# Kernel tuning notes

Hardware: AMD Instinct MI355X
Metric: run time of the kernel (lower is better)

Reference implementation:

```python
import jax, jax.numpy as jnp
import numpy as np

EMBED = 768
HEADS = 8
HEAD_DIM = EMBED // HEADS  # 96


def setup_inputs() -> dict:
    key = jax.random.key(0)
    k1, k2, k3, k4, k5 = jax.random.split(key, 5)
    b, n = 4, 2048
    x = jax.random.normal(k1, (b, n, EMBED), dtype=jnp.float32)
    s = 1.0 / np.sqrt(EMBED)
    W_qkv = jax.random.normal(k2, (EMBED, 3 * EMBED), dtype=jnp.float32) * s
    b_qkv = jax.random.normal(k3, (3 * EMBED,), dtype=jnp.float32) * 0.02
    W_proj = jax.random.normal(k4, (EMBED, EMBED), dtype=jnp.float32) * s
    b_proj = jax.random.normal(k5, (EMBED,), dtype=jnp.float32) * 0.02
    return {"x": x, "W_qkv": W_qkv, "b_qkv": b_qkv, "W_proj": W_proj, "b_proj": b_proj}


def reference(x, W_qkv, b_qkv, W_proj, b_proj):
    b, n, _ = x.shape
    qkv = x @ W_qkv + b_qkv  # [b, n, 3*EMBED]
    # rearrange 'b n (h d qkv) -> qkv b h n d': qkv is fastest-varying axis
    qkv = qkv.reshape(b, n, HEADS, HEAD_DIM, 3)
    q = jnp.transpose(qkv[..., 0], (0, 2, 1, 3))  # [b, h, n, d]
    k = jnp.transpose(qkv[..., 1], (0, 2, 1, 3))
    v = jnp.transpose(qkv[..., 2], (0, 2, 1, 3))
    scale = 1.0 / np.sqrt(HEAD_DIM)
    energy = jnp.einsum('bhqd,bhkd->bhqk', q, k) * scale
    attn = jax.nn.softmax(energy, axis=-1)  # dropout p=0 -> identity
    out = jnp.einsum('bhqk,bhkd->bhqd', attn, v)
    out = jnp.transpose(out, (0, 2, 1, 3)).reshape(b, n, EMBED)
    out = out @ W_proj + b_proj
    return out
```

## Files before the change

kernel.cpp:

```cpp
#include <hip/hip_runtime.h>
#include <hip/hip_bf16.h>

#define EMBED 768
#define NHEADS 8
#define HDIM 96
#define SEQ 2048
#define BATCH 4
#define NTOK (BATCH*SEQ)
#define QKVN (3*EMBED)

#define QSCALE 0.14724444f

typedef __attribute__((ext_vector_type(4))) float f32x4;
typedef __attribute__((ext_vector_type(8))) __bf16 bf16x8;

__device__ __forceinline__ unsigned short f2bf(float f) {
  union { float f; unsigned int u; } c; c.f = f;
  unsigned int u = c.u;
  return (unsigned short)((u + 0x7FFFu + ((u >> 16) & 1u)) >> 16);
}

__device__ __forceinline__ void gload_lds16(const void* g, void* l) {
  __builtin_amdgcn_global_load_lds(
      (const __attribute__((address_space(1))) unsigned int*)g,
      (__attribute__((address_space(3))) unsigned int*)l, 16, 0, 0);
}

__global__ __launch_bounds__(256) void cast_x_kernel(const float4* __restrict__ in,
                                                     ushort4* __restrict__ out, int n4) {
  int i = blockIdx.x * 256 + threadIdx.x;
  if (i >= n4) return;
  float4 v = in[i];
  out[i] = make_ushort4(f2bf(v.x), f2bf(v.y), f2bf(v.z), f2bf(v.w));
}

__global__ __launch_bounds__(256) void transpose_cast_kernel(const float* __restrict__ in,
                                                             unsigned short* __restrict__ out,
                                                             int R, int C) {
  __shared__ float t[32][33];
  int c0 = blockIdx.x * 32, r0 = blockIdx.y * 32;
  int tx = threadIdx.x & 31, ty = threadIdx.x >> 5;
  #pragma unroll
  for (int i = 0; i < 32; i += 8)
    t[ty + i][tx] = in[(size_t)(r0 + ty + i) * C + c0 + tx];
  __syncthreads();
  #pragma unroll
  for (int i = 0; i < 32; i += 8)
    out[(size_t)(c0 + ty + i) * R + r0 + tx] = f2bf(t[tx][ty + i]);
}

template <int MODE>
__global__ __launch_bounds__(256) void gemm_kernel(
    const unsigned short* __restrict__ A, const unsigned short* __restrict__ B,
    const float* __restrict__ bias, int K,
    unsigned short* __restrict__ Qo, unsigned short* __restrict__ Ko,
    unsigned short* __restrict__ Vt, float* __restrict__ out) {
  __shared__ unsigned short As[2][128][32];
  __shared__ unsigned short Bs[2][128][32];
  const int tid = threadIdx.x;
  const int lane = tid & 63, wid = tid >> 6;
  const int wr = wid >> 1, wc = wid & 1;
  const int l15 = lane & 15, l16 = lane >> 4;
  const int m0 = blockIdx.y * 128, n0 = blockIdx.x * 128;

  auto stage = [&](int buf, int k0) {
    #pragma unroll
    for (int i = 0; i < 2; i++) {
      int chunk = i * 256 + tid;
      gload_lds16(A + (size_t)(m0 + (chunk >> 2)) * K + k0 + (chunk & 3) * 8,
                  (char*)&As[buf][0][0] + (i * 256 + wid * 64) * 16);
      gload_lds16(B + (size_t)(n0 + (chunk >> 2)) * K + k0 + (chunk & 3) * 8,
                  (char*)&Bs[buf][0][0] + (i * 256 + wid * 64) * 16);
    }
  };

  f32x4 acc[4][4] = {};

  stage(0, 0);
  __syncthreads();
  int cur = 0;
  for (int k0 = 0; k0 < K; k0 += 32, cur ^= 1) {
    if (k0 + 32 < K) stage(cur ^ 1, k0 + 32);

    bf16x8 af[4], bfr[4];
    #pragma unroll
    for (int mi = 0; mi < 4; mi++)
      af[mi] = *(const bf16x8*)&As[cur][wr * 64 + mi * 16 + l15][l16 * 8];
    #pragma unroll
    for (int ni = 0; ni < 4; ni++)
      bfr[ni] = *(const bf16x8*)&Bs[cur][wc * 64 + ni * 16 + l15][l16 * 8];
    #pragma unroll
    for (int mi = 0; mi < 4; mi++)
      #pragma unroll
      for (int ni = 0; ni < 4; ni++)
        acc[mi][ni] = __builtin_amdgcn_mfma_f32_16x16x32_bf16(af[mi], bfr[ni], acc[mi][ni], 0, 0, 0);

    __syncthreads();
  }

  if (MODE == 0) {
    #pragma unroll
    for (int mi = 0; mi < 4; mi++) {
      #pragma unroll
      for (int ni = 0; ni < 4; ni++) {
        int col = n0 + wc * 64 + ni * 16 + l15;
        int h = col / 288;
        int rem = col - h * 288;
        int d = rem / 3;
        int which = rem - d * 3;
        float bb = bias[col];
        #pragma unroll
        for (int j = 0; j < 4; j++) {
          int row = m0 + wr * 64 + mi * 16 + l16 * 4 + j;
          int bi = row >> 11, nn = row & 2047;
          float v = acc[mi][ni][j] + bb;
          size_t bh = (size_t)(bi * NHEADS + h);
          if (which == 0)      Qo[(bh * SEQ + nn) * HDIM + d] = f2bf(v * QSCALE);
          else if (which == 1) Ko[(bh * SEQ + nn) * HDIM + d] = f2bf(v);
          else                 Vt[(bh * HDIM + d) * SEQ + nn] = f2bf(v);
        }
      }
    }
  } else {
    #pragma unroll
    for (int mi = 0; mi < 4; mi++) {
      #pragma unroll
      for (int ni = 0; ni < 4; ni++) {
        int col = n0 + wc * 64 + ni * 16 + l15;
        float bb = bias[col];
        #pragma unroll
        for (int j = 0; j < 4; j++) {
          int row = m0 + wr * 64 + mi * 16 + l16 * 4 + j;
          out[(size_t)row * EMBED + col] = acc[mi][ni][j] + bb;
        }
      }
    }
  }
}

__global__ __launch_bounds__(256) void attn_kernel(
    const unsigned short* __restrict__ Q, const unsigned short* __restrict__ Kd,
    const unsigned short* __restrict__ Vt, unsigned short* __restrict__ Oa) {
  __shared__ unsigned short Ks[64 * 96];
  __shared__ unsigned short Vs[96 * 64];
  __shared__ unsigned short Ps[4][32 * 64];

  const int tid = threadIdx.x, lane = tid & 63, wid = tid >> 6;
  const int l15 = lane & 15, l16 = lane >> 4;
  const int bid = blockIdx.x;
  const int swz = (bid & 7) * 64 + (bid >> 3);
  const int qb_ = swz & 15, bh = swz >> 4;
  const int bi = bh >> 3, h = bh & 7;
  const int q0 = qb_ * 128;

  const unsigned short* Qg = Q + ((size_t)bh * SEQ + q0) * HDIM;
  const unsigned short* Kg = Kd + (size_t)bh * SEQ * HDIM;
  const unsigned short* Vg = Vt + (size_t)bh * HDIM * SEQ;

  bf16x8 qf[2][3];
  #pragma unroll
  for (int qb = 0; qb < 2; qb++)
    #pragma unroll
    for (int ks = 0; ks < 3; ks++)
      qf[qb][ks] = *(const bf16x8*)(Qg + (size_t)(wid * 32 + qb * 16 + l15) * HDIM + ks * 32 + l16 * 8);

  auto stageKV = [&](int k0) {
    #pragma unroll
    for (int i = 0; i < 3; i++) {
      int idx = i * 256 + tid;
      gload_lds16(Kg + (size_t)k0 * HDIM + idx * 8,
                  (char*)Ks + (i * 256 + wid * 64) * 16);
    }
    #pragma unroll
    for (int i = 0; i < 3; i++) {
      int idx = i * 256 + tid;
      int d = idx >> 3, slot = idx & 7;
      gload_lds16(Vg + (size_t)d * SEQ + k0 + ((slot ^ (d & 7)) << 3),
                  (char*)Vs + (i * 256 + wid * 64) * 16);
    }
  };

  f32x4 oacc[2][6] = {};
  float mrow[2], lrow[2];
  mrow[0] = mrow[1] = -__builtin_inff();
  lrow[0] = lrow[1] = 0.f;

  char* pw = (char*)&Ps[wid][0];
  const int swzP = ((l15 & 7) << 4) ^ ((l15 & 8) << 2);

  for (int kb = 0; kb < SEQ / 64; kb++) {
    __syncthreads();
    stageKV(kb * 64);
    __syncthreads();

    f32x4 sacc[2][4] = {};
    #pragma unroll
    for (int ks = 0; ks < 3; ks++) {
      bf16x8 ak[4];
      #pragma unroll
      for (int ni = 0; ni < 4; ni++)
        ak[ni] = *(const bf16x8*)((const char*)Ks + (ni * 16 + l15) * 192 + ks * 64 + l16 * 16);
      #pragma unroll
      for (int qb = 0; qb < 2; qb++)
        #pragma unroll
        for (int ni = 0; ni < 4; ni++)
          sacc[qb][ni] = __builtin_amdgcn_mfma_f32_16x16x32_bf16(ak[ni], qf[qb][ks], sacc[qb][ni], 0, 0, 0);
    }

    float tmax[2];
    float g = -3.4e38f;
    #pragma unroll
    for (int qb = 0; qb < 2; qb++) {
      float v = fmaxf(
          fmaxf(fmaxf(fmaxf(sacc[qb][0][0], sacc[qb][0][1]), fmaxf(sacc[qb][0][2], sacc[qb][0][3])),
                fmaxf(fmaxf(sacc[qb][1][0], sacc[qb][1][1]), fmaxf(sacc[qb][1][2], sacc[qb][1][3]))),
          fmaxf(fmaxf(fmaxf(sacc[qb][2][0], sacc[qb][2][1]), fmaxf(sacc[qb][2][2], sacc[qb][2][3])),
                fmaxf(fmaxf(sacc[qb][3][0], sacc[qb][3][1]), fmaxf(sacc[qb][3][2], sacc[qb][3][3]))));
      v = fmaxf(v, __shfl_xor(v, 16));
      v = fmaxf(v, __shfl_xor(v, 32));
      tmax[qb] = v;
      g = fmaxf(g, v - mrow[qb]);
    }
    if (!__all(g <= 11.54f)) {
      #pragma unroll
      for (int qb = 0; qb < 2; qb++) {
        float mnew = fmaxf(mrow[qb], tmax[qb]);
        float alpha = __builtin_amdgcn_exp2f(mrow[qb] - mnew);
        mrow[qb] = mnew;
        lrow[qb] *= alpha;
        #pragma unroll
        for (int d6 = 0; d6 < 6; d6++) {
          oacc[qb][d6][0] *= alpha; oacc[qb][d6][1] *= alpha;
          oacc[qb][d6][2] *= alpha; oacc[qb][d6][3] *= alpha;
        }
      }
    }

    #pragma unroll
    for (int qb = 0; qb < 2; qb++) {
      const float m = mrow[qb];
      char* rowp = pw + (qb * 16 + l15) * 128;
      float psum = 0.f;
      #pragma unroll
      for (int ni = 0; ni < 4; ni++) {
        float p0 = __builtin_amdgcn_exp2f(sacc[qb][ni][0] - m);
        float p1 = __builtin_amdgcn_exp2f(sacc[qb][ni][1] - m);
        float p2 = __builtin_amdgcn_exp2f(sacc[qb][ni][2] - m);
        float p3 = __builtin_amdgcn_exp2f(sacc[qb][ni][3] - m);
        psum += (p0 + p1) + (p2 + p3);
        unsigned int w0 = (unsigned int)f2bf(p0) | ((unsigned int)f2bf(p1) << 16);
        unsigned int w1 = (unsigned int)f2bf(p2) | ((unsigned int)f2bf(p3) << 16);
        *(uint2*)(rowp + ((ni * 32 + l16 * 8) ^ swzP)) = make_uint2(w0, w1);
      }
      psum += __shfl_xor(psum, 16);
      psum += __shfl_xor(psum, 32);
      lrow[qb] += psum;
    }

    #pragma unroll
    for (int ks = 0; ks < 2; ks++) {
      bf16x8 pf[2], vb[6];
      #pragma unroll
      for (int qb = 0; qb < 2; qb++)
        pf[qb] = *(const bf16x8*)(pw + (qb * 16 + l15) * 128 + ((ks * 64 + l16 * 16) ^ swzP));
      #pragma unroll
      for (int d6 = 0; d6 < 6; d6++)
        vb[d6] = *(const bf16x8*)((const char*)Vs + (d6 * 16 + l15) * 128 +
                                  ((ks * 64 + l16 * 16) ^ ((l15 & 7) << 4)));
      #pragma unroll
      for (int qb = 0; qb < 2; qb++)
        #pragma unroll
        for (int d6 = 0; d6 < 6; d6++)
          oacc[qb][d6] = __builtin_amdgcn_mfma_f32_16x16x32_bf16(vb[d6], pf[qb], oacc[qb][d6], 0, 0, 0);
    }
  }

  #pragma unroll
  for (int qb = 0; qb < 2; qb++) {
    const float rl = 1.f / lrow[qb];
    const int tok = q0 + wid * 32 + qb * 16 + l15;
    unsigned short* Og = Oa + ((size_t)bi * SEQ + tok) * EMBED + h * HDIM;
    #pragma unroll
    for (int d6 = 0; d6 < 6; d6++) {
      ushort4 sv;
      sv.x = f2bf(oacc[qb][d6][0] * rl);
      sv.y = f2bf(oacc[qb][d6][1] * rl);
      sv.z = f2bf(oacc[qb][d6][2] * rl);
      sv.w = f2bf(oacc[qb][d6][3] * rl);
      *(ushort4*)(Og + d6 * 16 + l16 * 4) = sv;
    }
  }
}

extern "C" void kernel_launch(void* const* d_in, const int* in_sizes, int n_in,
                              void* d_out, int out_size, void* d_ws, size_t ws_size,
                              hipStream_t stream) {
  const float* x      = (const float*)d_in[0];
  const float* W_qkv  = (const float*)d_in[1];
  const float* b_qkv  = (const float*)d_in[2];
  const float* W_proj = (const float*)d_in[3];
  const float* b_proj = (const float*)d_in[4];
  float* out = (float*)d_out;

  char* ws = (char*)d_ws;
  size_t off = 0;
  auto alloc = [&](size_t bytes) { void* p = ws + off; off += (bytes + 255) & ~(size_t)255; return p; };
  unsigned short* xb  = (unsigned short*)alloc((size_t)NTOK * EMBED * 2);
  unsigned short* WqT = (unsigned short*)alloc((size_t)QKVN * EMBED * 2);
  unsigned short* WpT = (unsigned short*)alloc((size_t)EMBED * EMBED * 2);
  unsigned short* Qb  = (unsigned short*)alloc((size_t)NTOK * EMBED * 2);
  unsigned short* Kb  = (unsigned short*)alloc((size_t)NTOK * EMBED * 2);
  unsigned short* Vtb = (unsigned short*)alloc((size_t)NTOK * EMBED * 2);
  unsigned short* Ob  = (unsigned short*)alloc((size_t)NTOK * EMBED * 2);

  cast_x_kernel<<<dim3(NTOK * EMBED / 4 / 256), dim3(256), 0, stream>>>(
      (const float4*)x, (ushort4*)xb, NTOK * EMBED / 4);
  transpose_cast_kernel<<<dim3(QKVN / 32, EMBED / 32), dim3(256), 0, stream>>>(W_qkv, WqT, EMBED, QKVN);
  transpose_cast_kernel<<<dim3(EMBED / 32, EMBED / 32), dim3(256), 0, stream>>>(W_proj, WpT, EMBED, EMBED);

  gemm_kernel<0><<<dim3(QKVN / 128, NTOK / 128), dim3(256), 0, stream>>>(
      xb, WqT, b_qkv, EMBED, Qb, Kb, Vtb, nullptr);

  attn_kernel<<<dim3(BATCH * NHEADS * (SEQ / 128)), dim3(256), 0, stream>>>(Qb, Kb, Vtb, Ob);

  gemm_kernel<1><<<dim3(EMBED / 128, NTOK / 128), dim3(256), 0, stream>>>(
      Ob, WpT, b_proj, EMBED, nullptr, nullptr, nullptr, out);
}
```

Before: 187.2 us.

## Keep softmax probabilities in registers, double-buffer K/V, and regroup QKV weight columns

The QKV weight columns are reordered during the transpose-cast so each 16-column MFMA tile maps to one of Q/K/V and one head, which makes the epilogue stores contiguous. V is written in a permuted token order so that the packed P registers line up with the V fragments, removing the LDS round-trip for P. K/V tiles are double-buffered, so the load of the next tile overlaps compute and one barrier per iteration is dropped. Hardware packed bf16 conversion replaces the manual rounding. The permutation logic must match the MFMA register layout exactly, and the doubled K/V buffers increase LDS use, which may affect occupancy.

```diff
diff --git a/kernel.cpp b/kernel.cpp
--- a/kernel.cpp
+++ b/kernel.cpp
@@ -20,6 +20,12 @@
   return (unsigned short)((u + 0x7FFFu + ((u >> 16) & 1u)) >> 16);
 }
 
+__device__ __forceinline__ unsigned int cvt_pk_bf16(float lo, float hi) {
+  unsigned int r;
+  asm("v_cvt_pk_bf16_f32 %0, %1, %2" : "=v"(r) : "v"(lo), "v"(hi));
+  return r;
+}
+
 __device__ __forceinline__ void gload_lds16(const void* g, void* l) {
   __builtin_amdgcn_global_load_lds(
       (const __attribute__((address_space(1))) unsigned int*)g,
@@ -36,7 +42,7 @@
 
 __global__ __launch_bounds__(256) void transpose_cast_kernel(const float* __restrict__ in,
                                                              unsigned short* __restrict__ out,
-                                                             int R, int C) {
+                                                             int R, int C, int remap) {
   __shared__ float t[32][33];
   int c0 = blockIdx.x * 32, r0 = blockIdx.y * 32;
   int tx = threadIdx.x & 31, ty = threadIdx.x >> 5;
@@ -45,8 +51,11 @@
     t[ty + i][tx] = in[(size_t)(r0 + ty + i) * C + c0 + tx];
   __syncthreads();
   #pragma unroll
-  for (int i = 0; i < 32; i += 8)
-    out[(size_t)(c0 + ty + i) * R + r0 + tx] = f2bf(t[tx][ty + i]);
+  for (int i = 0; i < 32; i += 8) {
+    int c = c0 + ty + i;
+    int rp = remap ? (c % 3) * 768 + c / 3 : c;
+    out[(size_t)rp * R + r0 + tx] = f2bf(t[tx][ty + i]);
+  }
 }
 
 template <int MODE>
@@ -103,21 +112,24 @@
     for (int mi = 0; mi < 4; mi++) {
       #pragma unroll
       for (int ni = 0; ni < 4; ni++) {
-        int col = n0 + wc * 64 + ni * 16 + l15;
-        int h = col / 288;
-        int rem = col - h * 288;
-        int d = rem / 3;
-        int which = rem - d * 3;
-        float bb = bias[col];
+        int base = n0 + wc * 64 + ni * 16;
+        int which = base / 768;
+        int hd = base - which * 768;
+        int h = hd / 96;
+        int d0 = hd - h * 96;
+        float bb = bias[hd * 3 + which + 3 * l15];
         #pragma unroll
         for (int j = 0; j < 4; j++) {
           int row = m0 + wr * 64 + mi * 16 + l16 * 4 + j;
           int bi = row >> 11, nn = row & 2047;
           float v = acc[mi][ni][j] + bb;
           size_t bh = (size_t)(bi * NHEADS + h);
-          if (which == 0)      Qo[(bh * SEQ + nn) * HDIM + d] = f2bf(v * QSCALE);
-          else if (which == 1) Ko[(bh * SEQ + nn) * HDIM + d] = f2bf(v);
-          else                 Vt[(bh * HDIM + d) * SEQ + nn] = f2bf(v);
+          if (which == 0)      Qo[(bh * SEQ + nn) * HDIM + d0 + l15] = f2bf(v * QSCALE);
+          else if (which == 1) Ko[(bh * SEQ + nn) * HDIM + d0 + l15] = f2bf(v);
+          else {
+            int nn2 = (nn & ~63) | (nn & 32) | ((nn & 12) << 1) | ((nn & 16) >> 2) | (nn & 3);
+            Vt[(bh * HDIM + d0 + l15) * SEQ + nn2] = f2bf(v);
+          }
         }
       }
     }
@@ -141,9 +153,8 @@
 __global__ __launch_bounds__(256) void attn_kernel(
     const unsigned short* __restrict__ Q, const unsigned short* __restrict__ Kd,
     const unsigned short* __restrict__ Vt, unsigned short* __restrict__ Oa) {
-  __shared__ unsigned short Ks[64 * 96];
-  __shared__ unsigned short Vs[96 * 64];
-  __shared__ unsigned short Ps[4][32 * 64];
+  __shared__ unsigned short Ks[2][64 * 96];
+  __shared__ unsigned short Vs[2][96 * 64];
 
   const int tid = threadIdx.x, lane = tid & 63, wid = tid >> 6;
   const int l15 = lane & 15, l16 = lane >> 4;
@@ -164,19 +175,19 @@
     for (int ks = 0; ks < 3; ks++)
       qf[qb][ks] = *(const bf16x8*)(Qg + (size_t)(wid * 32 + qb * 16 + l15) * HDIM + ks * 32 + l16 * 8);
 
-  auto stageKV = [&](int k0) {
+  auto stageKV = [&](int buf, int k0) {
     #pragma unroll
     for (int i = 0; i < 3; i++) {
       int idx = i * 256 + tid;
       gload_lds16(Kg + (size_t)k0 * HDIM + idx * 8,
-                  (char*)Ks + (i * 256 + wid * 64) * 16);
+                  (char*)&Ks[buf][0] + (i * 256 + wid * 64) * 16);
     }
     #pragma unroll
     for (int i = 0; i < 3; i++) {
       int idx = i * 256 + tid;
-      int d = idx >> 3, slot = idx & 7;
-      gload_lds16(Vg + (size_t)d * SEQ + k0 + ((slot ^ (d & 7)) << 3),
-                  (char*)Vs + (i * 256 + wid * 64) * 16);
+      int d = idx >> 3, s = idx & 7;
+      gload_lds16(Vg + (size_t)d * SEQ + k0 + ((s ^ (d & 7)) << 3),
+                  (char*)&Vs[buf][0] + (i * 256 + wid * 64) * 16);
     }
   };
 
@@ -185,13 +196,15 @@
   mrow[0] = mrow[1] = -__builtin_inff();
   lrow[0] = lrow[1] = 0.f;
 
-  char* pw = (char*)&Ps[wid][0];
-  const int swzP = ((l15 & 7) << 4) ^ ((l15 & 8) << 2);
+  stageKV(0, 0);
+  __syncthreads();
 
   for (int kb = 0; kb < SEQ / 64; kb++) {
-    __syncthreads();
-    stageKV(kb * 64);
-    __syncthreads();
+    const int cur = kb & 1;
+    if (kb + 1 < SEQ / 64) stageKV(cur ^ 1, (kb + 1) * 64);
+
+    const char* Kc = (const char*)&Ks[cur][0];
+    const char* Vc = (const char*)&Vs[cur][0];
 
     f32x4 sacc[2][4] = {};
     #pragma unroll
@@ -199,7 +212,7 @@
       bf16x8 ak[4];
       #pragma unroll
       for (int ni = 0; ni < 4; ni++)
-        ak[ni] = *(const bf16x8*)((const char*)Ks + (ni * 16 + l15) * 192 + ks * 64 + l16 * 16);
+        ak[ni] = *(const bf16x8*)(Kc + (ni * 16 + l15) * 192 + ks * 64 + l16 * 16);
       #pragma unroll
       for (int qb = 0; qb < 2; qb++)
         #pragma unroll
@@ -211,11 +224,11 @@
     float g = -3.4e38f;
     #pragma unroll
     for (int qb = 0; qb < 2; qb++) {
-      float v = fmaxf(
-          fmaxf(fmaxf(fmaxf(sacc[qb][0][0], sacc[qb][0][1]), fmaxf(sacc[qb][0][2], sacc[qb][0][3])),
-                fmaxf(fmaxf(sacc[qb][1][0], sacc[qb][1][1]), fmaxf(sacc[qb][1][2], sacc[qb][1][3]))),
-          fmaxf(fmaxf(fmaxf(sacc[qb][2][0], sacc[qb][2][1]), fmaxf(sacc[qb][2][2], sacc[qb][2][3])),
-                fmaxf(fmaxf(sacc[qb][3][0], sacc[qb][3][1]), fmaxf(sacc[qb][3][2], sacc[qb][3][3]))));
+      float a0 = fmaxf(fmaxf(sacc[qb][0][0], sacc[qb][0][1]), fmaxf(sacc[qb][0][2], sacc[qb][0][3]));
+      float a1 = fmaxf(fmaxf(sacc[qb][1][0], sacc[qb][1][1]), fmaxf(sacc[qb][1][2], sacc[qb][1][3]));
+      float a2 = fmaxf(fmaxf(sacc[qb][2][0], sacc[qb][2][1]), fmaxf(sacc[qb][2][2], sacc[qb][2][3]));
+      float a3 = fmaxf(fmaxf(sacc[qb][3][0], sacc[qb][3][1]), fmaxf(sacc[qb][3][2], sacc[qb][3][3]));
+      float v = fmaxf(fmaxf(a0, a1), fmaxf(a2, a3));
       v = fmaxf(v, __shfl_xor(v, 16));
       v = fmaxf(v, __shfl_xor(v, 32));
       tmax[qb] = v;
@@ -236,10 +249,10 @@
       }
     }
 
+    unsigned int pk[2][8];
     #pragma unroll
     for (int qb = 0; qb < 2; qb++) {
       const float m = mrow[qb];
-      char* rowp = pw + (qb * 16 + l15) * 128;
       float psum = 0.f;
       #pragma unroll
       for (int ni = 0; ni < 4; ni++) {
@@ -248,9 +261,8 @@
         float p2 = __builtin_amdgcn_exp2f(sacc[qb][ni][2] - m);
         float p3 = __builtin_amdgcn_exp2f(sacc[qb][ni][3] - m);
         psum += (p0 + p1) + (p2 + p3);
-        unsigned int w0 = (unsigned int)f2bf(p0) | ((unsigned int)f2bf(p1) << 16);
-        unsigned int w1 = (unsigned int)f2bf(p2) | ((unsigned int)f2bf(p3) << 16);
-        *(uint2*)(rowp + ((ni * 32 + l16 * 8) ^ swzP)) = make_uint2(w0, w1);
+        pk[qb][ni * 2]     = cvt_pk_bf16(p0, p1);
+        pk[qb][ni * 2 + 1] = cvt_pk_bf16(p2, p3);
       }
       psum += __shfl_xor(psum, 16);
       psum += __shfl_xor(psum, 32);
@@ -259,20 +271,23 @@
 
     #pragma unroll
     for (int ks = 0; ks < 2; ks++) {
-      bf16x8 pf[2], vb[6];
-      #pragma unroll
-      for (int qb = 0; qb < 2; qb++)
-        pf[qb] = *(const bf16x8*)(pw + (qb * 16 + l15) * 128 + ((ks * 64 + l16 * 16) ^ swzP));
+      bf16x8 vb[6];
       #pragma unroll
       for (int d6 = 0; d6 < 6; d6++)
-        vb[d6] = *(const bf16x8*)((const char*)Vs + (d6 * 16 + l15) * 128 +
-                                  ((ks * 64 + l16 * 16) ^ ((l15 & 7) << 4)));
-      #pragma unroll
-      for (int qb = 0; qb < 2; qb++)
+        vb[d6] = *(const bf16x8*)(Vc + (d6 * 16 + l15) * 128 +
+                                  (((ks * 4 + l16) ^ (l15 & 7)) << 4));
+      #pragma unroll
+      for (int qb = 0; qb < 2; qb++) {
+        union { unsigned int u[4]; bf16x8 v; } pf;
+        pf.u[0] = pk[qb][4 * ks];     pf.u[1] = pk[qb][4 * ks + 1];
+        pf.u[2] = pk[qb][4 * ks + 2]; pf.u[3] = pk[qb][4 * ks + 3];
         #pragma unroll
         for (int d6 = 0; d6 < 6; d6++)
-          oacc[qb][d6] = __builtin_amdgcn_mfma_f32_16x16x32_bf16(vb[d6], pf[qb], oacc[qb][d6], 0, 0, 0);
-    }
+          oacc[qb][d6] = __builtin_amdgcn_mfma_f32_16x16x32_bf16(vb[d6], pf.v, oacc[qb][d6], 0, 0, 0);
+      }
+    }
+
+    __syncthreads();
   }
 
   #pragma unroll
@@ -282,12 +297,10 @@
     unsigned short* Og = Oa + ((size_t)bi * SEQ + tok) * EMBED + h * HDIM;
     #pragma unroll
     for (int d6 = 0; d6 < 6; d6++) {
-      ushort4 sv;
-      sv.x = f2bf(oacc[qb][d6][0] * rl);
-      sv.y = f2bf(oacc[qb][d6][1] * rl);
-      sv.z = f2bf(oacc[qb][d6][2] * rl);
-      sv.w = f2bf(oacc[qb][d6][3] * rl);
-      *(ushort4*)(Og + d6 * 16 + l16 * 4) = sv;
+      uint2 o;
+      o.x = cvt_pk_bf16(oacc[qb][d6][0] * rl, oacc[qb][d6][1] * rl);
+      o.y = cvt_pk_bf16(oacc[qb][d6][2] * rl, oacc[qb][d6][3] * rl);
+      *(uint2*)(Og + d6 * 16 + l16 * 4) = o;
     }
   }
 }
@@ -315,8 +328,8 @@
 
   cast_x_kernel<<<dim3(NTOK * EMBED / 4 / 256), dim3(256), 0, stream>>>(
       (const float4*)x, (ushort4*)xb, NTOK * EMBED / 4);
-  transpose_cast_kernel<<<dim3(QKVN / 32, EMBED / 32), dim3(256), 0, stream>>>(W_qkv, WqT, EMBED, QKVN);
-  transpose_cast_kernel<<<dim3(EMBED / 32, EMBED / 32), dim3(256), 0, stream>>>(W_proj, WpT, EMBED, EMBED);
+  transpose_cast_kernel<<<dim3(QKVN / 32, EMBED / 32), dim3(256), 0, stream>>>(W_qkv, WqT, EMBED, QKVN, 1);
+  transpose_cast_kernel<<<dim3(EMBED / 32, EMBED / 32), dim3(256), 0, stream>>>(W_proj, WpT, EMBED, EMBED, 0);
 
   gemm_kernel<0><<<dim3(QKVN / 128, NTOK / 128), dim3(256), 0, stream>>>(
       xb, WqT, b_qkv, EMBED, Qb, Kb, Vtb, nullptr);
```

Result: no change. 184.5 us (-1.5%).
